# Kernel optimization log

Hardware: AMD Instinct MI355X
Metric: run time of the kernel (lower is better)

The kernel has to match this reference:

```python
import jax, jax.numpy as jnp
import numpy as np

TEMPERATURE = 0.07
N, D = 8192, 1024
NUM_CLASSES = 1000


def setup_inputs() -> dict:
    key = jax.random.key(0)
    k1, k2 = jax.random.split(key)
    vectors = jax.random.normal(k1, (N, D), dtype=jnp.float32)
    labels = jax.random.randint(k2, (N,), 0, NUM_CLASSES, dtype=jnp.int32)
    return {"vectors": vectors, "labels": labels}


def reference(vectors, labels):
    # cosine similarity matrix, scaled by temperature
    a = vectors / jnp.linalg.norm(vectors, axis=1, keepdims=True)
    sim = jnp.matmul(a, a.T) / TEMPERATURE  # [N, N]
    n = sim.shape[0]
    eye = jnp.eye(n, dtype=bool)

    # per-row logsumexp over off-diagonal entries (diagonal removed)
    denom = jax.nn.logsumexp(jnp.where(eye, -jnp.inf, sim), axis=1)  # [N]

    # same-label mask, excluding self
    same = (labels[:, None] == labels[None, :]) & ~eye  # [N, N]
    cnt = jnp.sum(same, axis=1)  # [N] number of positives per anchor

    # numerator_j = -mean(sim[j, positives]); rows with no positives skipped
    pos_sum = jnp.sum(jnp.where(same, sim, 0.0), axis=1)
    numerator = -pos_sum / jnp.maximum(cnt, 1).astype(sim.dtype)

    per_row = jnp.where(cnt > 0, denom + numerator, 0.0)
    return jnp.sum(per_row)
```

## Files before the change

kernel.cpp:

```cpp
#include <hip/hip_runtime.h>
#include <hip/hip_bf16.h>
#include <stdint.h>

#define N_ROWS 8192
#define DIM    1024
#define INV_T  14.2857142857142857f
#define SCL    (INV_T / 1024.0f)

#define BM   128
#define RPB  512
#define TKB  64
#define NTILE  (N_ROWS / BM)
#define NSLICE (2 * NTILE)
#define NKT    8
#define NPAIR  2080
#define PER_XCD (NPAIR / 8)

typedef int   i32x4 __attribute__((ext_vector_type(4)));
typedef int   i32x8 __attribute__((ext_vector_type(8)));
typedef float f32x4 __attribute__((ext_vector_type(4)));

__device__ __forceinline__ unsigned e2m1(float y) {
    const float a = fabsf(y);
    unsigned c = a < 0.25f ? 0u : a < 0.75f ? 1u : a < 1.25f ? 2u :
                 a < 1.75f ? 3u : a < 2.5f  ? 4u : a < 3.5f  ? 5u :
                 a < 5.0f  ? 6u : 7u;
    return c | (y < 0.f ? 8u : 0u);
}

__global__ __launch_bounds__(256) void norm_kernel(
    const float* __restrict__ V, unsigned char* __restrict__ A4)
{
    const int wid  = threadIdx.x >> 6;
    const int lane = threadIdx.x & 63;
    const int row  = blockIdx.x * 4 + wid;

    const float4* vp = (const float4*)(V + (size_t)row * DIM);
    float4 v[4];
    float ss = 0.f;
    #pragma unroll
    for (int i = 0; i < 4; ++i) {
        v[i] = vp[lane + i * 64];
        ss += v[i].x*v[i].x + v[i].y*v[i].y + v[i].z*v[i].z + v[i].w*v[i].w;
    }
    #pragma unroll
    for (int off = 1; off < 64; off <<= 1) ss += __shfl_xor(ss, off, 64);
    const float inv = 32.0f / sqrtf(ss);

    ushort4 o;
    unsigned short* op = (unsigned short*)&o;
    #pragma unroll
    for (int i = 0; i < 4; ++i) {
        const unsigned e0 = e2m1(v[i].x * inv), e1 = e2m1(v[i].y * inv);
        const unsigned e2 = e2m1(v[i].z * inv), e3 = e2m1(v[i].w * inv);
        op[i] = (unsigned short)(e0 | (e1 << 4) | (e2 << 8) | (e3 << 12));
    }
    unsigned char* dst = A4 + (size_t)row * RPB;
    #pragma unroll
    for (int i = 0; i < 4; ++i)
        ((unsigned short*)dst)[lane + i * 64] = op[i];
}

__global__ __launch_bounds__(256, 3) void sim_kernel(
    const unsigned char* __restrict__ A4, const int* __restrict__ labels,
    float* __restrict__ psum, float* __restrict__ ppos, float* __restrict__ pcnt)
{
    __shared__ __align__(16) unsigned char As[2][BM * TKB];
    __shared__ __align__(16) unsigned char Bs[2][BM * TKB];

    const int b = blockIdx.x;
    const int v = (b & 7) * PER_XCD + (b >> 3);
    int rem = v, RT = 0, rowsz = 36 + 7 * 64;
    while (rem >= rowsz) { rem -= rowsz; ++RT; rowsz -= 64; }
    int rt, ct;
    if (rem < 36) {
        int i = 0, left = 8;
        while (rem >= left) { rem -= left; ++i; --left; }
        rt = RT * 8 + i;  ct = RT * 8 + i + rem;
    } else {
        const int o  = rem - 36;
        const int CT = RT + 1 + (o >> 6);
        const int w  = o & 63;
        rt = RT * 8 + (w >> 3);
        ct = CT * 8 + (w & 7);
    }
    const bool isDiag = (rt == ct);

    const int tid  = threadIdx.x;
    const int lane = tid & 63;
    const int wid  = tid >> 6;
    const int wr   = wid >> 1;
    const int wc   = wid & 1;

    const int rbase = rt * BM;
    const int cbase = ct * BM;

    const int t = lane >> 4;
    const int j = lane & 15;

    const int rowq = rbase + wr * 64 + (t << 2);
    const int col0 = cbase + wc * 64 + j;

    int labr[16];
    #pragma unroll
    for (int m = 0; m < 4; ++m)
        #pragma unroll
        for (int r = 0; r < 4; ++r)
            labr[m * 4 + r] = labels[rowq + m * 16 + r];
    int labc[4];
    #pragma unroll
    for (int n = 0; n < 4; ++n) labc[n] = labels[col0 + n * 16];

    f32x4 acc[4][4];
    #pragma unroll
    for (int m = 0; m < 4; ++m)
        #pragma unroll
        for (int n = 0; n < 4; ++n)
            acc[m][n] = (f32x4){0.f, 0.f, 0.f, 0.f};

    #define STAGE(buf, kt)                                                         \
    {                                                                              \
        const int kbase = (kt) * TKB;                                              \
        _Pragma("unroll")                                                          \
        for (int i = 0; i < 2; ++i) {                                              \
            const int c    = i * 256 + tid;                                        \
            const int rowc = c >> 2;                                               \
            const int kcs  = (c & 3) ^ (rowc & 3);                                 \
            const unsigned char* gA = A4 + (size_t)(rbase + rowc) * RPB + kbase + kcs * 16; \
            const unsigned char* gB = A4 + (size_t)(cbase + rowc) * RPB + kbase + kcs * 16; \
            const int ldsOff = i * 4096 + wid * 1024;          \
            __builtin_amdgcn_global_load_lds(                                      \
                (const __attribute__((address_space(1))) void*)gA,                 \
                (__attribute__((address_space(3))) void*)(As[buf] + ldsOff),       \
                16, 0, 0);                                                         \
            __builtin_amdgcn_global_load_lds(                                      \
                (const __attribute__((address_space(1))) void*)gB,                 \
                (__attribute__((address_space(3))) void*)(Bs[buf] + ldsOff),       \
                16, 0, 0);                                                         \
        }                                                                          \
    }

    const i32x4 Z4 = (i32x4){0, 0, 0, 0};

    STAGE(0, 0);
    __syncthreads();

    int cur = 0;
    for (int kt = 0; kt < NKT; ++kt) {
        i32x8 a8[4], b8[4];
        #pragma unroll
        for (int m = 0; m < 4; ++m) {
            const int rowa = wr * 64 + m * 16 + j;
            const int ph   = ((t ^ (rowa & 3)) << 4);
            i32x4 q = *(const i32x4*)(As[cur] + rowa * TKB + ph);
            a8[m] = __builtin_shufflevector(q, Z4, 0, 1, 2, 3, 4, 5, 6, 7);
        }
        #pragma unroll
        for (int n = 0; n < 4; ++n) {
            const int rowb = wc * 64 + n * 16 + j;
            const int ph   = ((t ^ (rowb & 3)) << 4);
            i32x4 q = *(const i32x4*)(Bs[cur] + rowb * TKB + ph);
            b8[n] = __builtin_shufflevector(q, Z4, 0, 1, 2, 3, 4, 5, 6, 7);
        }

        if (kt + 1 < NKT) STAGE(cur ^ 1, kt + 1);

        __builtin_amdgcn_s_setprio(1);
        #pragma unroll
        for (int m = 0; m < 4; ++m)
            #pragma unroll
            for (int n = 0; n < 4; ++n)
                acc[m][n] = __builtin_amdgcn_mfma_scale_f32_16x16x128_f8f6f4(
                    a8[m], b8[n], acc[m][n],
                    4 , 4 ,
                    0, 0x7F , 0, 0x7F );
        __builtin_amdgcn_s_setprio(0);

        __syncthreads();
        cur ^= 1;
    }

    float sum_p[16], pos_p[16], cnt_p[16];
    #pragma unroll
    for (int i = 0; i < 16; ++i) { sum_p[i] = 0.f; pos_p[i] = 0.f; cnt_p[i] = 0.f; }
    float csum[4], cpos[4], ccnt[4];
    #pragma unroll
    for (int n = 0; n < 4; ++n) { csum[n] = 0.f; cpos[n] = 0.f; ccnt[n] = 0.f; }

    if (isDiag) {
        #pragma unroll
        for (int m = 0; m < 4; ++m)
            #pragma unroll
            for (int n = 0; n < 4; ++n) {
                const int gcol = col0 + n * 16;
                #pragma unroll
                for (int r = 0; r < 4; ++r) {
                    const float s    = acc[m][n][r] * SCL;
                    const int   i16  = m * 4 + r;
                    const int   grow = rowq + m * 16 + r;
                    const bool  diag = (grow == gcol);
                    sum_p[i16] += diag ? 0.f : __expf(s);
                    if ((labr[i16] == labc[n]) && !diag) {
                        pos_p[i16] += s; cnt_p[i16] += 1.f;
                    }
                }
            }
    } else {
        #pragma unroll
        for (int m = 0; m < 4; ++m)
            #pragma unroll
            for (int n = 0; n < 4; ++n) {
                #pragma unroll
                for (int r = 0; r < 4; ++r) {
                    const float s   = acc[m][n][r] * SCL;
                    const int   i16 = m * 4 + r;
                    const float e   = __expf(s);
                    sum_p[i16] += e;
                    csum[n]    += e;
                    if (labr[i16] == labc[n]) {
                        pos_p[i16] += s; cnt_p[i16] += 1.f;
                        cpos[n]    += s; ccnt[n]    += 1.f;
                    }
                }
            }
    }

    #pragma unroll
    for (int bb = 1; bb <= 8; bb <<= 1) {
        const bool hi = (j & bb) != 0;
        #pragma unroll
        for (int k = 0; k < 8; ++k) {
            if (k < 16 / (2 * bb)) {
                const float eK = hi ? sum_p[2*k+1] : sum_p[2*k];
                const float eS = hi ? sum_p[2*k]   : sum_p[2*k+1];
                sum_p[k] = eK + __shfl_xor(eS, bb, 16);
                const float pK = hi ? pos_p[2*k+1] : pos_p[2*k];
                const float pS = hi ? pos_p[2*k]   : pos_p[2*k+1];
                pos_p[k] = pK + __shfl_xor(pS, bb, 16);
                const float cK = hi ? cnt_p[2*k+1] : cnt_p[2*k];
                const float cS = hi ? cnt_p[2*k]   : cnt_p[2*k+1];
                cnt_p[k] = cK + __shfl_xor(cS, bb, 16);
            }
        }
    }
    {
        const int rowS = rowq + ((j >> 2) << 4) + (j & 3);
        const size_t idx = (size_t)(ct * 2 + wc) * N_ROWS + rowS;
        psum[idx] = sum_p[0];
        ppos[idx] = pos_p[0];
        pcnt[idx] = cnt_p[0];
    }

    if (!isDiag) {
        #pragma unroll
        for (int n = 0; n < 4; ++n) {
            float se = csum[n], pp = cpos[n], cc = ccnt[n];
            se += __shfl_xor(se, 16, 64); se += __shfl_xor(se, 32, 64);
            pp += __shfl_xor(pp, 16, 64); pp += __shfl_xor(pp, 32, 64);
            cc += __shfl_xor(cc, 16, 64); cc += __shfl_xor(cc, 32, 64);
            if (lane < 16) {
                const int gcol = col0 + n * 16;
                const size_t idx = (size_t)(rt * 2 + wr) * N_ROWS + gcol;
                psum[idx] = se;
                ppos[idx] = pp;
                pcnt[idx] = cc;
            }
        }
    }
}

__global__ __launch_bounds__(256) void finalize_kernel(
    const float* __restrict__ psum, const float* __restrict__ ppos,
    const float* __restrict__ pcnt, float* __restrict__ out)
{
    const int row  = blockIdx.x * 256 + threadIdx.x;
    const int lane = threadIdx.x & 63, wid = threadIdx.x >> 6;

    float s = 0.f, p = 0.f, c = 0.f;
    #pragma unroll 8
    for (int sl = 0; sl < NSLICE; ++sl) {
        const size_t idx = (size_t)sl * N_ROWS + row;
        s += psum[idx];
        p += ppos[idx];
        c += pcnt[idx];
    }
    float per = (c > 0.f) ? (logf(s) - p / c) : 0.f;
    #pragma unroll
    for (int off = 32; off > 0; off >>= 1) per += __shfl_down(per, off, 64);
    __shared__ float w4[4];
    if (lane == 0) w4[wid] = per;
    __syncthreads();
    if (threadIdx.x == 0)
        atomicAdd(out, w4[0] + w4[1] + w4[2] + w4[3]);
}

extern "C" void kernel_launch(void* const* d_in, const int* in_sizes, int n_in,
                              void* d_out, int out_size, void* d_ws, size_t ws_size,
                              hipStream_t stream) {
    const float* V      = (const float*)d_in[0];
    const int*   labels = (const int*)d_in[1];
    float*       out    = (float*)d_out;

    unsigned char* A4 = (unsigned char*)d_ws;
    char* base = (char*)d_ws + (size_t)N_ROWS * RPB;
    float* psum = (float*)(base);
    float* ppos = (float*)(base + (size_t)NSLICE * N_ROWS * 4);
    float* pcnt = (float*)(base + (size_t)NSLICE * N_ROWS * 8);

    hipMemsetAsync(out, 0, sizeof(float), stream);
    norm_kernel<<<N_ROWS / 4, 256, 0, stream>>>(V, A4);
    sim_kernel<<<NPAIR, 256, 0, stream>>>(A4, labels, psum, ppos, pcnt);
    finalize_kernel<<<N_ROWS / 256, 256, 0, stream>>>(psum, ppos, pcnt, out);
}
```

Before: 64.60 us.

## Load GEMM operands directly into registers, split finalize slices across more threads

The sim kernel no longer stages A/B tiles through LDS with global_load_lds and block barriers. Each lane now loads its own 16-byte operand fragments straight from global memory into a two-deep register double buffer, with the K loop fully unrolled. This removes the LDS round-trip and the per-iteration __syncthreads, but it gives up cross-wave sharing of loaded data, so global and L2 traffic rise and register pressure grows. The finalize kernel also uses 1024 threads per block, each summing a quarter of the slices before an LDS reduction, to expose more memory parallelism.

```diff
diff --git a/kernel.cpp b/kernel.cpp
--- a/kernel.cpp
+++ b/kernel.cpp
@@ -47,8 +47,7 @@
     for (int off = 1; off < 64; off <<= 1) ss += __shfl_xor(ss, off, 64);
     const float inv = 32.0f / sqrtf(ss);
 
-    ushort4 o;
-    unsigned short* op = (unsigned short*)&o;
+    unsigned short op[4];
     #pragma unroll
     for (int i = 0; i < 4; ++i) {
         const unsigned e0 = e2m1(v[i].x * inv), e1 = e2m1(v[i].y * inv);
@@ -65,9 +64,6 @@
     const unsigned char* __restrict__ A4, const int* __restrict__ labels,
     float* __restrict__ psum, float* __restrict__ ppos, float* __restrict__ pcnt)
 {
-    __shared__ __align__(16) unsigned char As[2][BM * TKB];
-    __shared__ __align__(16) unsigned char Bs[2][BM * TKB];
-
     const int b = blockIdx.x;
     const int v = (b & 7) * PER_XCD + (b >> 3);
     int rem = v, RT = 0, rowsz = 36 + 7 * 64;
@@ -111,6 +107,15 @@
     #pragma unroll
     for (int n = 0; n < 4; ++n) labc[n] = labels[col0 + n * 16];
 
+    const unsigned char* pa[4];
+    const unsigned char* pb[4];
+    #pragma unroll
+    for (int m = 0; m < 4; ++m)
+        pa[m] = A4 + (size_t)(rbase + wr * 64 + m * 16 + j) * RPB + t * 16;
+    #pragma unroll
+    for (int n = 0; n < 4; ++n)
+        pb[n] = A4 + (size_t)(cbase + wc * 64 + n * 16 + j) * RPB + t * 16;
+
     f32x4 acc[4][4];
     #pragma unroll
     for (int m = 0; m < 4; ++m)
@@ -118,66 +123,39 @@
         for (int n = 0; n < 4; ++n)
             acc[m][n] = (f32x4){0.f, 0.f, 0.f, 0.f};
 
-    #define STAGE(buf, kt)                                                         \
-    {                                                                              \
-        const int kbase = (kt) * TKB;                                              \
-        _Pragma("unroll")                                                          \
-        for (int i = 0; i < 2; ++i) {                                              \
-            const int c    = i * 256 + tid;                                        \
-            const int rowc = c >> 2;                                               \
-            const int kcs  = (c & 3) ^ (rowc & 3);                                 \
-            const unsigned char* gA = A4 + (size_t)(rbase + rowc) * RPB + kbase + kcs * 16; \
-            const unsigned char* gB = A4 + (size_t)(cbase + rowc) * RPB + kbase + kcs * 16; \
-            const int ldsOff = i * 4096 + wid * 1024;          \
-            __builtin_amdgcn_global_load_lds(                                      \
-                (const __attribute__((address_space(1))) void*)gA,                 \
-                (__attribute__((address_space(3))) void*)(As[buf] + ldsOff),       \
-                16, 0, 0);                                                         \
-            __builtin_amdgcn_global_load_lds(                                      \
-                (const __attribute__((address_space(1))) void*)gB,                 \
-                (__attribute__((address_space(3))) void*)(Bs[buf] + ldsOff),       \
-                16, 0, 0);                                                         \
-        }                                                                          \
-    }
-
     const i32x4 Z4 = (i32x4){0, 0, 0, 0};
-
-    STAGE(0, 0);
-    __syncthreads();
-
-    int cur = 0;
+    i32x4 fa[2][4], fb[2][4];
+
+    #pragma unroll
+    for (int m = 0; m < 4; ++m) fa[0][m] = *(const i32x4*)(pa[m]);
+    #pragma unroll
+    for (int n = 0; n < 4; ++n) fb[0][n] = *(const i32x4*)(pb[n]);
+
+    #pragma unroll
     for (int kt = 0; kt < NKT; ++kt) {
-        i32x8 a8[4], b8[4];
+        const int cur = kt & 1;
+        if (kt + 1 < NKT) {
+            #pragma unroll
+            for (int m = 0; m < 4; ++m)
+                fa[cur ^ 1][m] = *(const i32x4*)(pa[m] + (kt + 1) * TKB);
+            #pragma unroll
+            for (int n = 0; n < 4; ++n)
+                fb[cur ^ 1][n] = *(const i32x4*)(pb[n] + (kt + 1) * TKB);
+        }
+        __builtin_amdgcn_s_setprio(1);
         #pragma unroll
         for (int m = 0; m < 4; ++m) {
-            const int rowa = wr * 64 + m * 16 + j;
-            const int ph   = ((t ^ (rowa & 3)) << 4);
-            i32x4 q = *(const i32x4*)(As[cur] + rowa * TKB + ph);
-            a8[m] = __builtin_shufflevector(q, Z4, 0, 1, 2, 3, 4, 5, 6, 7);
-        }
-        #pragma unroll
-        for (int n = 0; n < 4; ++n) {
-            const int rowb = wc * 64 + n * 16 + j;
-            const int ph   = ((t ^ (rowb & 3)) << 4);
-            i32x4 q = *(const i32x4*)(Bs[cur] + rowb * TKB + ph);
-            b8[n] = __builtin_shufflevector(q, Z4, 0, 1, 2, 3, 4, 5, 6, 7);
-        }
-
-        if (kt + 1 < NKT) STAGE(cur ^ 1, kt + 1);
-
-        __builtin_amdgcn_s_setprio(1);
-        #pragma unroll
-        for (int m = 0; m < 4; ++m)
-            #pragma unroll
-            for (int n = 0; n < 4; ++n)
+            const i32x8 a8 = __builtin_shufflevector(fa[cur][m], Z4, 0,1,2,3,4,5,6,7);
+            #pragma unroll
+            for (int n = 0; n < 4; ++n) {
+                const i32x8 b8 = __builtin_shufflevector(fb[cur][n], Z4, 0,1,2,3,4,5,6,7);
                 acc[m][n] = __builtin_amdgcn_mfma_scale_f32_16x16x128_f8f6f4(
-                    a8[m], b8[n], acc[m][n],
+                    a8, b8, acc[m][n],
                     4 , 4 ,
                     0, 0x7F , 0, 0x7F );
+            }
+        }
         __builtin_amdgcn_s_setprio(0);
-
-        __syncthreads();
-        cur ^= 1;
     }
 
     float sum_p[16], pos_p[16], cnt_p[16];
@@ -269,28 +247,41 @@
     }
 }
 
-__global__ __launch_bounds__(256) void finalize_kernel(
+__global__ __launch_bounds__(1024) void finalize_kernel(
     const float* __restrict__ psum, const float* __restrict__ ppos,
     const float* __restrict__ pcnt, float* __restrict__ out)
 {
-    const int row  = blockIdx.x * 256 + threadIdx.x;
-    const int lane = threadIdx.x & 63, wid = threadIdx.x >> 6;
+    __shared__ float sh0[1024], sh1[1024], sh2[1024];
+    __shared__ float w4[4];
+
+    const int tid = threadIdx.x;
+    const int r   = tid & 255;
+    const int q   = tid >> 8;
+    const int row = blockIdx.x * 256 + r;
 
     float s = 0.f, p = 0.f, c = 0.f;
     #pragma unroll 8
-    for (int sl = 0; sl < NSLICE; ++sl) {
+    for (int sl = q * 32; sl < q * 32 + 32; ++sl) {
         const size_t idx = (size_t)sl * N_ROWS + row;
         s += psum[idx];
         p += ppos[idx];
         c += pcnt[idx];
     }
-    float per = (c > 0.f) ? (logf(s) - p / c) : 0.f;
+    sh0[tid] = s; sh1[tid] = p; sh2[tid] = c;
+    __syncthreads();
+
+    float per = 0.f;
+    if (tid < 256) {
+        s = sh0[tid] + sh0[tid + 256] + sh0[tid + 512] + sh0[tid + 768];
+        p = sh1[tid] + sh1[tid + 256] + sh1[tid + 512] + sh1[tid + 768];
+        c = sh2[tid] + sh2[tid + 256] + sh2[tid + 512] + sh2[tid + 768];
+        per = (c > 0.f) ? (logf(s) - p / c) : 0.f;
+    }
     #pragma unroll
     for (int off = 32; off > 0; off >>= 1) per += __shfl_down(per, off, 64);
-    __shared__ float w4[4];
-    if (lane == 0) w4[wid] = per;
+    if (tid < 256 && (tid & 63) == 0) w4[tid >> 6] = per;
     __syncthreads();
-    if (threadIdx.x == 0)
+    if (tid == 0)
         atomicAdd(out, w4[0] + w4[1] + w4[2] + w4[3]);
 }
 
@@ -310,5 +301,5 @@
     hipMemsetAsync(out, 0, sizeof(float), stream);
     norm_kernel<<<N_ROWS / 4, 256, 0, stream>>>(V, A4);
     sim_kernel<<<NPAIR, 256, 0, stream>>>(A4, labels, psum, ppos, pcnt);
-    finalize_kernel<<<N_ROWS / 256, 256, 0, stream>>>(psum, ppos, pcnt, out);
-}
+    finalize_kernel<<<N_ROWS / 256, 1024, 0, stream>>>(psum, ppos, pcnt, out);
+}
```

Measured after the change: 98.21 us. 1.52x slower.
